# Optimization experiments

Hardware: AMD Instinct MI355X
Metric: run time of the kernel (lower is better)

Reference implementation:

```python
import jax, jax.numpy as jnp
import numpy as np

B, F, MP, P = 4, 9, 100, 12000   # batch, point feats, max_points, max_pillars
C = 64                            # nb_channels
NY = NX = 400                     # canvas
EPS = 1e-3
POOL_W = 100                      # encoder MaxPool2d kernel (1, max_points)


def setup_inputs() -> dict:
    key = jax.random.key(0)
    ks = jax.random.split(key, 12)
    x = jax.random.normal(ks[0], (B, F, MP, P), dtype=jnp.float32)
    # coords[:, 0]=batch id, [:,2]=y, [:,3]=x ; unique (y,x) per batch so scatter is well-defined
    rng = np.random.default_rng(0)
    coords = np.zeros((B * P, 4), dtype=np.int32)
    for b in range(B):
        lin = rng.choice(NY * NX, size=P, replace=False)
        coords[b * P:(b + 1) * P, 0] = b
        coords[b * P:(b + 1) * P, 2] = lin // NX
        coords[b * P:(b + 1) * P, 3] = lin % NX
    coords = jnp.asarray(coords)
    w1 = jax.random.normal(ks[1], (C, F), dtype=jnp.float32) * 0.1
    b1 = jax.random.normal(ks[2], (C,), dtype=jnp.float32) * 0.1
    g1 = 1.0 + 0.1 * jax.random.normal(ks[3], (C,), dtype=jnp.float32)
    be1 = 0.1 * jax.random.normal(ks[4], (C,), dtype=jnp.float32)
    m1 = 0.1 * jax.random.normal(ks[5], (C,), dtype=jnp.float32)
    v1 = 0.5 + jax.random.uniform(ks[6], (C,), dtype=jnp.float32)
    w2 = jax.random.normal(ks[7], (C, C), dtype=jnp.float32) * 0.1
    b2 = jax.random.normal(ks[8], (C,), dtype=jnp.float32) * 0.1
    g2 = 1.0 + 0.1 * jax.random.normal(ks[9], (C,), dtype=jnp.float32)
    be2 = 0.1 * jax.random.normal(ks[10], (C,), dtype=jnp.float32)
    m2 = 0.1 * jax.random.normal(ks[11], (C,), dtype=jnp.float32)
    v2 = 0.5 + jax.random.uniform(jax.random.fold_in(key, 99), (C,), dtype=jnp.float32)
    return {"x": x, "coords": coords, "w1": w1, "b1": b1, "g1": g1, "be1": be1,
            "m1": m1, "v1": v1, "w2": w2, "b2": b2, "g2": g2, "be2": be2,
            "m2": m2, "v2": v2}


def _bn_scale_shift(g, be, m, v):
    s = g * jax.lax.rsqrt(v + EPS)
    return s, be - m * s


def reference(x, coords, w1, b1, g1, be1, m1, v1, w2, b2, g2, be2, m2, v2):
    # ---- MiniPointNet: conv1x1 + BN(eval) + ReLU + maxpool over points ----
    s1, t1 = _bn_scale_shift(g1, be1, m1, v1)
    h = jnp.einsum('bfhw,cf->bchw', x, w1) + b1[None, :, None, None]
    h = jax.nn.relu(h * s1[None, :, None, None] + t1[None, :, None, None])
    feat = jnp.max(h, axis=2)                       # [B, C, P]
    # ---- PointPillarsScatter (vectorized over batch) ----
    voxels = feat.transpose(0, 2, 1).reshape(B * P, C)   # [B*P, C]
    flat = (coords[:, 0].astype(jnp.int32) * (NY * NX)
            + coords[:, 2].astype(jnp.int32) * NX
            + coords[:, 3].astype(jnp.int32))
    canvas = jnp.zeros((B * NY * NX, C), dtype=voxels.dtype).at[flat].set(voxels)
    canvas = canvas.reshape(B, NY, NX, C).transpose(0, 3, 1, 2)  # [B, C, NY, NX]
    # ---- BackBoneEncoder: conv1x1 + BN(eval) + ReLU + maxpool (1, POOL_W) ----
    s2, t2 = _bn_scale_shift(g2, be2, m2, v2)
    h2 = jnp.einsum('bchw,dc->bdhw', canvas, w2) + b2[None, :, None, None]
    h2 = jax.nn.relu(h2 * s2[None, :, None, None] + t2[None, :, None, None])
    out = jnp.max(h2.reshape(B, C, NY, NX // POOL_W, POOL_W), axis=-1)  # [B,C,NY,NX/100]
    return out
```

## Files before the change

kernel.cpp:

```cpp
#include <hip/hip_runtime.h>
#include <hip/hip_bf16.h>

#define BB   4
#define FF   9
#define MPP  100
#define PP   12000
#define CC   64
#define NYY  400
#define NXO  4
#define NPIL (BB * PP)
#define NWIN (BB * NYY * NXO)

#define WS_CNT    0
#define WS_BINS   36352
#define WS_FEAT2  (WS_BINS + 1280000)

typedef __attribute__((ext_vector_type(8)))  short short8;
typedef __attribute__((ext_vector_type(16))) float float16;
typedef __attribute__((ext_vector_type(4)))  unsigned short ushort4v;

__device__ __forceinline__ short f2bf(float v) {
    __hip_bfloat16 h = __float2bfloat16(v);
    short s; __builtin_memcpy(&s, &h, 2); return s;
}
__device__ __forceinline__ float bf2f(unsigned short u) {
    return __int_as_float(((int)u) << 16);
}
__device__ __forceinline__ int fkey(float v) {
    int b = __float_as_int(v);
    return b >= 0 ? b : (b ^ 0x7fffffff);
}
__device__ __forceinline__ float kinv(int k) {
    return __int_as_float(k >= 0 ? k : (k ^ 0x7fffffff));
}

#define LOAD5(dst, ptr) do { \
    dst##0 = __builtin_nontemporal_load((ptr)); \
    dst##1 = __builtin_nontemporal_load((ptr) + FS); \
    dst##2 = __builtin_nontemporal_load((ptr) + 2 * FS); \
    dst##3 = __builtin_nontemporal_load((ptr) + 3 * FS); \
    dst##4 = __builtin_nontemporal_load((ptr) + off4); } while (0)

#define BUILD_BF(bf, s_) do { \
    bf[0] = f2bf(s_##0); bf[1] = f2bf(s_##1); bf[2] = f2bf(s_##2); \
    bf[3] = f2bf(s_##3); bf[4] = half ? f2bf(s_##4) : (short)0; } while (0)

#define STEP2(sA, sB) do { \
    short8 bfA = (short8)0, bfB = (short8)0; \
    BUILD_BF(bfA, sA); BUILD_BF(bfB, sB); \
    const float16 z0A = __builtin_amdgcn_mfma_f32_32x32x16_bf16(af0, bfA, (float16)0.f, 0, 0, 0); \
    const float16 z1A = __builtin_amdgcn_mfma_f32_32x32x16_bf16(af1, bfA, (float16)0.f, 0, 0, 0); \
    const float16 z0B = __builtin_amdgcn_mfma_f32_32x32x16_bf16(af0, bfB, (float16)0.f, 0, 0, 0); \
    const float16 z1B = __builtin_amdgcn_mfma_f32_32x32x16_bf16(af1, bfB, (float16)0.f, 0, 0, 0); \
    _Pragma("unroll") \
    for (int r = 0; r < 16; ++r) { \
        vmx0[r] = fmaxf(fmaxf(vmx0[r], z0A[r]), z0B[r]); \
        vmx1[r] = fmaxf(fmaxf(vmx1[r], z1A[r]), z1B[r]); \
    } } while (0)

__global__ __launch_bounds__(256, 4) void pillar_kernel(
    const float* __restrict__ x, const int* __restrict__ coords,
    const float* __restrict__ w1, const float* __restrict__ b1,
    const float* __restrict__ g1, const float* __restrict__ be1,
    const float* __restrict__ m1, const float* __restrict__ v1,
    const float* __restrict__ w2, const float* __restrict__ b2,
    const float* __restrict__ g2, const float* __restrict__ be2,
    const float* __restrict__ m2, const float* __restrict__ v2,
    char* __restrict__ ws, int* __restrict__ cnt)
{
    __shared__ char  arena[8448];
    __shared__ short featbT[32 * 72];
    __shared__ short w1pb_s[64 * 16];
    __shared__ short w2pb_s[64 * 80];
    __shared__ float bias1_s[64];
    __shared__ float bias2_s[64];

    int*   red = (int*)arena;
    float* s2f = (float*)arena;

    unsigned short* bins  = (unsigned short*)(ws + WS_BINS);
    short*          feat2 = (short*)(ws + WS_FEAT2);

    const int t    = threadIdx.x;
    const int lane = t & 63;
    const int wv   = t >> 6;
    const int half = lane >> 5;
    const int pcol = lane & 31;
    const int v0   = blockIdx.x * 32;
    const int b    = v0 / PP;
    const int p0   = v0 - b * PP;

    #pragma unroll
    for (int i = 0; i < 8; ++i) red[i * 256 + t] = (int)0x80000000;

    if (t < 32) {
        const int* c4 = coords + (size_t)(v0 + t) * 4;
        const int w = (c4[0] * NYY + c4[2]) * NXO + c4[3] / 100;
        const int slot = atomicAdd(&cnt[w], 1);
        bins[w * 100 + slot] = (unsigned short)(v0 + t);
    }

    if (t < 64) {
        const float s1 = g1[t] * rsqrtf(v1[t] + 1e-3f);
        bias1_s[t] = s1 * b1[t] + (be1[t] - m1[t] * s1);
        #pragma unroll
        for (int s = 0; s < 16; ++s) {
            const int f = (s < 4) ? s : ((s >= 8 && s < 13) ? s - 4 : -1);
            w1pb_s[t * 16 + s] = (f >= 0) ? f2bf(s1 * w1[t * 9 + f]) : (short)0;
        }
        const float s2 = g2[t] * rsqrtf(v2[t] + 1e-3f);
        bias2_s[t] = s2 * b2[t] + (be2[t] - m2[t] * s2);
    }
    #pragma unroll
    for (int i0 = 0; i0 < 16; ++i0) {
        const int i = i0 * 256 + t;
        const int d = i >> 6;
        const float s2d = g2[d] * rsqrtf(v2[d] + 1e-3f);
        w2pb_s[d * 80 + (i & 63)] = f2bf(s2d * w2[i]);
    }
    __syncthreads();

    const short8 af0 = *(const short8*)(w1pb_s + pcol * 16 + half * 8);
    const short8 af1 = *(const short8*)(w1pb_s + (pcol + 32) * 16 + half * 8);

    float16 vmx0, vmx1;
    #pragma unroll
    for (int r = 0; r < 16; ++r) { vmx0[r] = -3.0e38f; vmx1[r] = -3.0e38f; }

    const size_t FS = (size_t)MPP * PP;
    const size_t off4 = (size_t)(half ? 4 : 3) * FS;
    const float* q = x + (size_t)b * FF * FS
                       + (size_t)(wv * 25) * PP
                       + (size_t)half * 4 * FS
                       + p0 + pcol;

    float a_0, a_1, a_2, a_3, a_4, b_0, b_1, b_2, b_3, b_4;
    float c_0, c_1, c_2, c_3, c_4, d_0, d_1, d_2, d_3, d_4;
    LOAD5(a_, q); LOAD5(b_, q + PP); q += 2 * PP;
    LOAD5(c_, q); LOAD5(d_, q + PP); q += 2 * PP;

    for (int it = 0; it < 10; ++it) {
        float n0_0, n0_1, n0_2, n0_3, n0_4, n1_0, n1_1, n1_2, n1_3, n1_4;
        LOAD5(n0_, q); LOAD5(n1_, q + PP); q += 2 * PP;
        STEP2(a_, b_);
        a_0 = c_0; a_1 = c_1; a_2 = c_2; a_3 = c_3; a_4 = c_4;
        b_0 = d_0; b_1 = d_1; b_2 = d_2; b_3 = d_3; b_4 = d_4;
        c_0 = n0_0; c_1 = n0_1; c_2 = n0_2; c_3 = n0_3; c_4 = n0_4;
        d_0 = n1_0; d_1 = n1_1; d_2 = n1_2; d_3 = n1_3; d_4 = n1_4;
    }
    STEP2(a_, b_);
    STEP2(c_, d_);
    {
        LOAD5(a_, q);
        short8 bfA = (short8)0;
        BUILD_BF(bfA, a_);
        const float16 z0 = __builtin_amdgcn_mfma_f32_32x32x16_bf16(af0, bfA, (float16)0.f, 0, 0, 0);
        const float16 z1 = __builtin_amdgcn_mfma_f32_32x32x16_bf16(af1, bfA, (float16)0.f, 0, 0, 0);
        #pragma unroll
        for (int r = 0; r < 16; ++r) {
            vmx0[r] = fmaxf(vmx0[r], z0[r]);
            vmx1[r] = fmaxf(vmx1[r], z1[r]);
        }
    }

    #pragma unroll
    for (int r = 0; r < 16; ++r) {
        const int chl = (r & 3) + 8 * (r >> 2) + 4 * half;
        atomicMax(&red[chl * 32 + pcol],        fkey(vmx0[r]));
        atomicMax(&red[(chl + 32) * 32 + pcol], fkey(vmx1[r]));
    }
    __syncthreads();

    {
        const int p  = t & 31;
        const int cg = t >> 5;
        #pragma unroll
        for (int j = 0; j < 8; ++j) {
            const int c = cg * 8 + j;
            const float m = kinv(red[c * 32 + p]);
            featbT[p * 72 + c] = f2bf(fmaxf(0.f, m + bias1_s[c]));
        }
    }
    __syncthreads();

    if (wv < 2) {
        const short* wrow = &w2pb_s[(wv * 32 + pcol) * 80 + half * 8];
        const short8 wa0 = *(const short8*)(wrow +  0);
        const short8 wa1 = *(const short8*)(wrow + 16);
        const short8 wa2 = *(const short8*)(wrow + 32);
        const short8 wa3 = *(const short8*)(wrow + 48);
        const short* frow = &featbT[pcol * 72 + half * 8];
        const short8 fb0 = *(const short8*)(frow +  0);
        const short8 fb1 = *(const short8*)(frow + 16);
        const short8 fb2 = *(const short8*)(frow + 32);
        const short8 fb3 = *(const short8*)(frow + 48);

        float16 acc = (float16)0.f;
        acc = __builtin_amdgcn_mfma_f32_32x32x16_bf16(wa0, fb0, acc, 0, 0, 0);
        acc = __builtin_amdgcn_mfma_f32_32x32x16_bf16(wa1, fb1, acc, 0, 0, 0);
        acc = __builtin_amdgcn_mfma_f32_32x32x16_bf16(wa2, fb2, acc, 0, 0, 0);
        acc = __builtin_amdgcn_mfma_f32_32x32x16_bf16(wa3, fb3, acc, 0, 0, 0);

        #pragma unroll
        for (int r = 0; r < 16; ++r) {
            const int d = wv * 32 + (r & 3) + 8 * (r >> 2) + 4 * half;
            s2f[pcol * 66 + d] = fmaxf(0.f, acc[r] + bias2_s[d]);
        }
    }
    __syncthreads();

    {
        const int p  = t >> 3;
        const int d0 = (t & 7) * 8;
        short8 o;
        #pragma unroll
        for (int j = 0; j < 8; ++j) o[j] = f2bf(s2f[p * 66 + d0 + j]);
        *(short8*)(feat2 + (size_t)(v0 + p) * 64 + d0) = o;
    }
}

__global__ __launch_bounds__(256) void gather_kernel(
    const float* __restrict__ g2, const float* __restrict__ b2,
    const float* __restrict__ be2, const float* __restrict__ m2,
    const float* __restrict__ v2,
    const char* __restrict__ ws, const int* __restrict__ cnt,
    float* __restrict__ out)
{
    const unsigned short* bins  = (const unsigned short*)(ws + WS_BINS);
    const unsigned short* feat2 = (const unsigned short*)(ws + WS_FEAT2);

    const int t  = threadIdx.x;
    const int wl = t & 63;
    const int dg = t >> 6;
    const int w  = blockIdx.x * 64 + wl;
    const int k  = cnt[w];

    float m[16];
    #pragma unroll
    for (int j = 0; j < 16; ++j) {
        const int d = dg * 16 + j;
        const float s2 = g2[d] * rsqrtf(v2[d] + 1e-3f);
        const float bias2d = s2 * b2[d] + (be2[d] - m2[d] * s2);
        const float zv = fmaxf(0.f, bias2d);
        m[j] = (k >= 100) ? 0.f : zv;
    }

    const unsigned short* brow = bins + (size_t)w * 100;
    for (int i = 0; i < k; i += 4) {
        const ushort4v p4 = *(const ushort4v*)(brow + i);
        #pragma unroll
        for (int j = 0; j < 4; ++j) {
            if (i + j < k) {
                const unsigned short* row = feat2 + (size_t)p4[j] * 64 + dg * 16;
                const short8 a0 = *(const short8*)(row);
                const short8 a1 = *(const short8*)(row + 8);
                #pragma unroll
                for (int jj = 0; jj < 8; ++jj) {
                    m[jj]     = fmaxf(m[jj],     bf2f((unsigned short)a0[jj]));
                    m[jj + 8] = fmaxf(m[jj + 8], bf2f((unsigned short)a1[jj]));
                }
            }
        }
    }

    const int b   = w / (NYY * NXO);
    const int rem = w - b * (NYY * NXO);
    const int y   = rem >> 2;
    const int xo  = rem & 3;
    #pragma unroll
    for (int j = 0; j < 16; ++j) {
        const int d = dg * 16 + j;
        out[(((size_t)b * CC + d) * NYY + y) * NXO + xo] = m[j];
    }
}

extern "C" void kernel_launch(void* const* d_in, const int* in_sizes, int n_in,
                              void* d_out, int out_size, void* d_ws, size_t ws_size,
                              hipStream_t stream) {
    const float* x   = (const float*)d_in[0];
    const int*   cds = (const int*)d_in[1];
    const float* w1  = (const float*)d_in[2];
    const float* b1  = (const float*)d_in[3];
    const float* g1  = (const float*)d_in[4];
    const float* be1 = (const float*)d_in[5];
    const float* m1  = (const float*)d_in[6];
    const float* v1  = (const float*)d_in[7];
    const float* w2  = (const float*)d_in[8];
    const float* b2  = (const float*)d_in[9];
    const float* g2  = (const float*)d_in[10];
    const float* be2 = (const float*)d_in[11];
    const float* m2  = (const float*)d_in[12];
    const float* v2  = (const float*)d_in[13];

    char* ws = (char*)d_ws;
    int*  cnt = (int*)(ws + WS_CNT);

    hipMemsetAsync(cnt, 0, (size_t)NWIN * 4, stream);

    pillar_kernel<<<NPIL / 32, 256, 0, stream>>>(x, cds,
                                                 w1, b1, g1, be1, m1, v1,
                                                 w2, b2, g2, be2, m2, v2,
                                                 ws, cnt);

    gather_kernel<<<NWIN / 64, 256, 0, stream>>>(g2, b2, be2, m2, v2,
                                                 ws, cnt, (float*)d_out);
}
```

Baseline: 274.7 us.

## Load all 9 features per lane, permlane-swap into MFMA operands, 64 pillars per block

The pillar kernel now has each lane load all nine features for one pillar across 64 pillars per block. It packs them to bf16 and uses v_permlane32_swap to build the MFMA B operands, instead of splitting features across lane halves for 32 pillars. This widens the coalesced load footprint and doubles the MFMA work per block, and the second conv now uses all four waves. The gather kernel moves from one thread per window to one wave per window, with lanes striding over bins and a shuffle max reduction, to balance irregular bin lengths. Occupancy hint drops to 3 blocks and LDS use grows.

```diff
diff --git a/kernel.cpp b/kernel.cpp
--- a/kernel.cpp
+++ b/kernel.cpp
@@ -17,7 +17,7 @@
 
 typedef __attribute__((ext_vector_type(8)))  short short8;
 typedef __attribute__((ext_vector_type(16))) float float16;
-typedef __attribute__((ext_vector_type(4)))  unsigned short ushort4v;
+typedef __attribute__((ext_vector_type(4)))  int int4v;
 
 __device__ __forceinline__ short f2bf(float v) {
     __hip_bfloat16 h = __float2bfloat16(v);
@@ -33,32 +33,51 @@
 __device__ __forceinline__ float kinv(int k) {
     return __int_as_float(k >= 0 ? k : (k ^ 0x7fffffff));
 }
-
-#define LOAD5(dst, ptr) do { \
-    dst##0 = __builtin_nontemporal_load((ptr)); \
-    dst##1 = __builtin_nontemporal_load((ptr) + FS); \
-    dst##2 = __builtin_nontemporal_load((ptr) + 2 * FS); \
-    dst##3 = __builtin_nontemporal_load((ptr) + 3 * FS); \
-    dst##4 = __builtin_nontemporal_load((ptr) + off4); } while (0)
-
-#define BUILD_BF(bf, s_) do { \
-    bf[0] = f2bf(s_##0); bf[1] = f2bf(s_##1); bf[2] = f2bf(s_##2); \
-    bf[3] = f2bf(s_##3); bf[4] = half ? f2bf(s_##4) : (short)0; } while (0)
-
-#define STEP2(sA, sB) do { \
-    short8 bfA = (short8)0, bfB = (short8)0; \
-    BUILD_BF(bfA, sA); BUILD_BF(bfB, sB); \
-    const float16 z0A = __builtin_amdgcn_mfma_f32_32x32x16_bf16(af0, bfA, (float16)0.f, 0, 0, 0); \
-    const float16 z1A = __builtin_amdgcn_mfma_f32_32x32x16_bf16(af1, bfA, (float16)0.f, 0, 0, 0); \
-    const float16 z0B = __builtin_amdgcn_mfma_f32_32x32x16_bf16(af0, bfB, (float16)0.f, 0, 0, 0); \
-    const float16 z1B = __builtin_amdgcn_mfma_f32_32x32x16_bf16(af1, bfB, (float16)0.f, 0, 0, 0); \
+__device__ __forceinline__ unsigned pack2(float lo, float hi) {
+    unsigned a = (unsigned short)f2bf(lo);
+    unsigned b = (unsigned short)f2bf(hi);
+    return a | (b << 16);
+}
+__device__ __forceinline__ void pls(unsigned &a, unsigned &b) {
+    asm volatile("v_permlane32_swap_b32 %0, %1" : "+v"(a), "+v"(b));
+}
+__device__ __forceinline__ short8 mk8(unsigned a, unsigned b, unsigned c) {
+    int4v t; t[0] = (int)a; t[1] = (int)b; t[2] = (int)c; t[3] = 0;
+    short8 r; __builtin_memcpy(&r, &t, 16); return r;
+}
+
+#define LOAD9(g, mp_) do { \
+    const float* bp_ = xq + (size_t)(mp_) * PP; \
+    g##0 = __builtin_nontemporal_load(bp_ + loff); \
+    g##1 = __builtin_nontemporal_load(bp_ + 1 * FS + loff); \
+    g##2 = __builtin_nontemporal_load(bp_ + 2 * FS + loff); \
+    g##3 = __builtin_nontemporal_load(bp_ + 3 * FS + loff); \
+    g##4 = __builtin_nontemporal_load(bp_ + 4 * FS + loff); \
+    g##5 = __builtin_nontemporal_load(bp_ + 5 * FS + loff); \
+    g##6 = __builtin_nontemporal_load(bp_ + 6 * FS + loff); \
+    g##7 = __builtin_nontemporal_load(bp_ + 7 * FS + loff); \
+    g##8 = __builtin_nontemporal_load(bp_ + 8 * FS + loff); } while (0)
+
+#define STEPP(g) do { \
+    unsigned p01 = pack2(g##0, g##1), p23 = pack2(g##2, g##3); \
+    unsigned p45 = pack2(g##4, g##5), p67 = pack2(g##6, g##7); \
+    unsigned p8z = pack2(g##8, 0.f);  unsigned zz = 0u; \
+    pls(p01, p45); pls(p23, p67); pls(zz, p8z); \
+    const short8 fr0 = mk8(p01, p23, zz); \
+    const short8 fr1 = mk8(p45, p67, p8z); \
+    const float16 zA = __builtin_amdgcn_mfma_f32_32x32x16_bf16(af0, fr0, (float16)0.f, 0, 0, 0); \
+    const float16 zB = __builtin_amdgcn_mfma_f32_32x32x16_bf16(af1, fr0, (float16)0.f, 0, 0, 0); \
+    const float16 zC = __builtin_amdgcn_mfma_f32_32x32x16_bf16(af0, fr1, (float16)0.f, 0, 0, 0); \
+    const float16 zD = __builtin_amdgcn_mfma_f32_32x32x16_bf16(af1, fr1, (float16)0.f, 0, 0, 0); \
     _Pragma("unroll") \
     for (int r = 0; r < 16; ++r) { \
-        vmx0[r] = fmaxf(fmaxf(vmx0[r], z0A[r]), z0B[r]); \
-        vmx1[r] = fmaxf(fmaxf(vmx1[r], z1A[r]), z1B[r]); \
+        vmx00[r] = fmaxf(vmx00[r], zA[r]); \
+        vmx10[r] = fmaxf(vmx10[r], zB[r]); \
+        vmx01[r] = fmaxf(vmx01[r], zC[r]); \
+        vmx11[r] = fmaxf(vmx11[r], zD[r]); \
     } } while (0)
 
-__global__ __launch_bounds__(256, 4) void pillar_kernel(
+__global__ __launch_bounds__(256, 3) void pillar_kernel(
     const float* __restrict__ x, const int* __restrict__ coords,
     const float* __restrict__ w1, const float* __restrict__ b1,
     const float* __restrict__ g1, const float* __restrict__ be1,
@@ -68,8 +87,8 @@
     const float* __restrict__ m2, const float* __restrict__ v2,
     char* __restrict__ ws, int* __restrict__ cnt)
 {
-    __shared__ char  arena[8448];
-    __shared__ short featbT[32 * 72];
+    __shared__ char  arena[16896];
+    __shared__ short featbT[64 * 72];
     __shared__ short w1pb_s[64 * 16];
     __shared__ short w2pb_s[64 * 80];
     __shared__ float bias1_s[64];
@@ -86,14 +105,12 @@
     const int wv   = t >> 6;
     const int half = lane >> 5;
     const int pcol = lane & 31;
-    const int v0   = blockIdx.x * 32;
-    const int b    = v0 / PP;
-    const int p0   = v0 - b * PP;
-
-    #pragma unroll
-    for (int i = 0; i < 8; ++i) red[i * 256 + t] = (int)0x80000000;
-
-    if (t < 32) {
+    const int v0   = blockIdx.x * 64;
+
+    #pragma unroll
+    for (int i = 0; i < 16; ++i) red[i * 256 + t] = (int)0x80000000;
+
+    if (t < 64) {
         const int* c4 = coords + (size_t)(v0 + t) * 4;
         const int w = (c4[0] * NYY + c4[2]) * NXO + c4[3] / 100;
         const int slot = atomicAdd(&cnt[w], 1);
@@ -123,73 +140,60 @@
     const short8 af0 = *(const short8*)(w1pb_s + pcol * 16 + half * 8);
     const short8 af1 = *(const short8*)(w1pb_s + (pcol + 32) * 16 + half * 8);
 
-    float16 vmx0, vmx1;
-    #pragma unroll
-    for (int r = 0; r < 16; ++r) { vmx0[r] = -3.0e38f; vmx1[r] = -3.0e38f; }
+    float16 vmx00, vmx10, vmx01, vmx11;
+    #pragma unroll
+    for (int r = 0; r < 16; ++r) {
+        vmx00[r] = -3.0e38f; vmx10[r] = -3.0e38f;
+        vmx01[r] = -3.0e38f; vmx11[r] = -3.0e38f;
+    }
 
     const size_t FS = (size_t)MPP * PP;
-    const size_t off4 = (size_t)(half ? 4 : 3) * FS;
-    const float* q = x + (size_t)b * FF * FS
-                       + (size_t)(wv * 25) * PP
-                       + (size_t)half * 4 * FS
-                       + p0 + pcol;
-
-    float a_0, a_1, a_2, a_3, a_4, b_0, b_1, b_2, b_3, b_4;
-    float c_0, c_1, c_2, c_3, c_4, d_0, d_1, d_2, d_3, d_4;
-    LOAD5(a_, q); LOAD5(b_, q + PP); q += 2 * PP;
-    LOAD5(c_, q); LOAD5(d_, q + PP); q += 2 * PP;
-
-    for (int it = 0; it < 10; ++it) {
-        float n0_0, n0_1, n0_2, n0_3, n0_4, n1_0, n1_1, n1_2, n1_3, n1_4;
-        LOAD5(n0_, q); LOAD5(n1_, q + PP); q += 2 * PP;
-        STEP2(a_, b_);
-        a_0 = c_0; a_1 = c_1; a_2 = c_2; a_3 = c_3; a_4 = c_4;
-        b_0 = d_0; b_1 = d_1; b_2 = d_2; b_3 = d_3; b_4 = d_4;
-        c_0 = n0_0; c_1 = n0_1; c_2 = n0_2; c_3 = n0_3; c_4 = n0_4;
-        d_0 = n1_0; d_1 = n1_1; d_2 = n1_2; d_3 = n1_3; d_4 = n1_4;
-    }
-    STEP2(a_, b_);
-    STEP2(c_, d_);
-    {
-        LOAD5(a_, q);
-        short8 bfA = (short8)0;
-        BUILD_BF(bfA, a_);
-        const float16 z0 = __builtin_amdgcn_mfma_f32_32x32x16_bf16(af0, bfA, (float16)0.f, 0, 0, 0);
-        const float16 z1 = __builtin_amdgcn_mfma_f32_32x32x16_bf16(af1, bfA, (float16)0.f, 0, 0, 0);
-        #pragma unroll
-        for (int r = 0; r < 16; ++r) {
-            vmx0[r] = fmaxf(vmx0[r], z0[r]);
-            vmx1[r] = fmaxf(vmx1[r], z1[r]);
-        }
-    }
+    const int pid = v0 + lane;
+    const int bl  = pid / PP;
+    const int loff = bl * (int)(FF * FS) + (pid - bl * PP);
+    const float* xq = x + (size_t)(wv * 25) * PP;
+
+    float a_0, a_1, a_2, a_3, a_4, a_5, a_6, a_7, a_8;
+    float b_0, b_1, b_2, b_3, b_4, b_5, b_6, b_7, b_8;
+    for (int it = 0; it < 12; ++it) {
+        LOAD9(a_, 2 * it);
+        LOAD9(b_, 2 * it + 1);
+        STEPP(a_);
+        STEPP(b_);
+    }
+    LOAD9(a_, 24);
+    STEPP(a_);
 
     #pragma unroll
     for (int r = 0; r < 16; ++r) {
         const int chl = (r & 3) + 8 * (r >> 2) + 4 * half;
-        atomicMax(&red[chl * 32 + pcol],        fkey(vmx0[r]));
-        atomicMax(&red[(chl + 32) * 32 + pcol], fkey(vmx1[r]));
+        atomicMax(&red[chl * 64 + pcol],             fkey(vmx00[r]));
+        atomicMax(&red[(chl + 32) * 64 + pcol],      fkey(vmx10[r]));
+        atomicMax(&red[chl * 64 + 32 + pcol],        fkey(vmx01[r]));
+        atomicMax(&red[(chl + 32) * 64 + 32 + pcol], fkey(vmx11[r]));
     }
     __syncthreads();
 
     {
-        const int p  = t & 31;
-        const int cg = t >> 5;
-        #pragma unroll
-        for (int j = 0; j < 8; ++j) {
-            const int c = cg * 8 + j;
-            const float m = kinv(red[c * 32 + p]);
+        const int p  = t & 63;
+        const int cg = t >> 6;
+        #pragma unroll
+        for (int j = 0; j < 16; ++j) {
+            const int c = cg * 16 + j;
+            const float m = kinv(red[c * 64 + p]);
             featbT[p * 72 + c] = f2bf(fmaxf(0.f, m + bias1_s[c]));
         }
     }
     __syncthreads();
 
-    if (wv < 2) {
-        const short* wrow = &w2pb_s[(wv * 32 + pcol) * 80 + half * 8];
+    {
+        const int dt = wv & 1, pt = wv >> 1;
+        const short* wrow = &w2pb_s[(dt * 32 + pcol) * 80 + half * 8];
         const short8 wa0 = *(const short8*)(wrow +  0);
         const short8 wa1 = *(const short8*)(wrow + 16);
         const short8 wa2 = *(const short8*)(wrow + 32);
         const short8 wa3 = *(const short8*)(wrow + 48);
-        const short* frow = &featbT[pcol * 72 + half * 8];
+        const short* frow = &featbT[(pt * 32 + pcol) * 72 + half * 8];
         const short8 fb0 = *(const short8*)(frow +  0);
         const short8 fb1 = *(const short8*)(frow + 16);
         const short8 fb2 = *(const short8*)(frow + 32);
@@ -203,19 +207,23 @@
 
         #pragma unroll
         for (int r = 0; r < 16; ++r) {
-            const int d = wv * 32 + (r & 3) + 8 * (r >> 2) + 4 * half;
-            s2f[pcol * 66 + d] = fmaxf(0.f, acc[r] + bias2_s[d]);
+            const int d = dt * 32 + (r & 3) + 8 * (r >> 2) + 4 * half;
+            s2f[(pt * 32 + pcol) * 66 + d] = fmaxf(0.f, acc[r] + bias2_s[d]);
         }
     }
     __syncthreads();
 
     {
-        const int p  = t >> 3;
-        const int d0 = (t & 7) * 8;
-        short8 o;
-        #pragma unroll
-        for (int j = 0; j < 8; ++j) o[j] = f2bf(s2f[p * 66 + d0 + j]);
-        *(short8*)(feat2 + (size_t)(v0 + p) * 64 + d0) = o;
+        const int p  = t >> 2;
+        const int d0 = (t & 3) * 16;
+        short8 o0, o1;
+        #pragma unroll
+        for (int j = 0; j < 8; ++j) {
+            o0[j] = f2bf(s2f[p * 66 + d0 + j]);
+            o1[j] = f2bf(s2f[p * 66 + d0 + 8 + j]);
+        }
+        *(short8*)(feat2 + (size_t)(v0 + p) * 64 + d0)     = o0;
+        *(short8*)(feat2 + (size_t)(v0 + p) * 64 + d0 + 8) = o1;
     }
 }
 
@@ -229,11 +237,13 @@
     const unsigned short* bins  = (const unsigned short*)(ws + WS_BINS);
     const unsigned short* feat2 = (const unsigned short*)(ws + WS_FEAT2);
 
-    const int t  = threadIdx.x;
-    const int wl = t & 63;
-    const int dg = t >> 6;
-    const int w  = blockIdx.x * 64 + wl;
-    const int k  = cnt[w];
+    const int t    = threadIdx.x;
+    const int lane = t & 63;
+    const int wv   = t >> 6;
+    const int w    = blockIdx.x * 4 + wv;
+    const int dg   = lane & 3;
+    const int cc   = lane >> 2;
+    const int k    = cnt[w];
 
     float m[16];
     #pragma unroll
@@ -246,31 +256,35 @@
     }
 
     const unsigned short* brow = bins + (size_t)w * 100;
-    for (int i = 0; i < k; i += 4) {
-        const ushort4v p4 = *(const ushort4v*)(brow + i);
-        #pragma unroll
-        for (int j = 0; j < 4; ++j) {
-            if (i + j < k) {
-                const unsigned short* row = feat2 + (size_t)p4[j] * 64 + dg * 16;
-                const short8 a0 = *(const short8*)(row);
-                const short8 a1 = *(const short8*)(row + 8);
-                #pragma unroll
-                for (int jj = 0; jj < 8; ++jj) {
-                    m[jj]     = fmaxf(m[jj],     bf2f((unsigned short)a0[jj]));
-                    m[jj + 8] = fmaxf(m[jj + 8], bf2f((unsigned short)a1[jj]));
-                }
-            }
-        }
-    }
-
-    const int b   = w / (NYY * NXO);
-    const int rem = w - b * (NYY * NXO);
-    const int y   = rem >> 2;
-    const int xo  = rem & 3;
-    #pragma unroll
-    for (int j = 0; j < 16; ++j) {
-        const int d = dg * 16 + j;
-        out[(((size_t)b * CC + d) * NYY + y) * NXO + xo] = m[j];
+    for (int i = cc; i < k; i += 16) {
+        const int pid = brow[i];
+        const unsigned short* row = feat2 + (size_t)pid * 64 + dg * 16;
+        const short8 a0 = *(const short8*)(row);
+        const short8 a1 = *(const short8*)(row + 8);
+        #pragma unroll
+        for (int j = 0; j < 8; ++j) {
+            m[j]     = fmaxf(m[j],     bf2f((unsigned short)a0[j]));
+            m[j + 8] = fmaxf(m[j + 8], bf2f((unsigned short)a1[j]));
+        }
+    }
+
+    #pragma unroll
+    for (int off = 4; off < 64; off <<= 1) {
+        #pragma unroll
+        for (int j = 0; j < 16; ++j)
+            m[j] = fmaxf(m[j], __shfl_xor(m[j], off, 64));
+    }
+
+    if (cc == 0) {
+        const int b   = w / (NYY * NXO);
+        const int rem = w - b * (NYY * NXO);
+        const int y   = rem >> 2;
+        const int xo  = rem & 3;
+        #pragma unroll
+        for (int j = 0; j < 16; ++j) {
+            const int d = dg * 16 + j;
+            out[(((size_t)b * CC + d) * NYY + y) * NXO + xo] = m[j];
+        }
     }
 }
 
@@ -297,11 +311,11 @@
 
     hipMemsetAsync(cnt, 0, (size_t)NWIN * 4, stream);
 
-    pillar_kernel<<<NPIL / 32, 256, 0, stream>>>(x, cds,
+    pillar_kernel<<<NPIL / 64, 256, 0, stream>>>(x, cds,
                                                  w1, b1, g1, be1, m1, v1,
                                                  w2, b2, g2, be2, m2, v2,
                                                  ws, cnt);
 
-    gather_kernel<<<NWIN / 64, 256, 0, stream>>>(g2, b2, be2, m2, v2,
-                                                 ws, cnt, (float*)d_out);
-}
+    gather_kernel<<<NWIN / 4, 256, 0, stream>>>(g2, b2, be2, m2, v2,
+                                                ws, cnt, (float*)d_out);
+}
```

After: 274.9 us. No clear change (+0.1%).
